# Performance work log

Hardware: AMD Instinct MI355X
Metric: run time of the kernel (lower is better)

The kernel has to match this reference:

```python
import jax, jax.numpy as jnp
import numpy as np
import math

B, S, H = 1, 2048, 4096
NH, HD = 32, 128  # heads, head_dim
ROPE_THETA = 10000.0
SINK = 4
RECENT_RATIO = 0.1


def setup_inputs() -> dict:
    key = jax.random.key(0)
    ks = jax.random.split(key, 5)
    scale = 0.02
    return {
        "hidden_states": jax.random.normal(ks[0], (B, S, H), jnp.float32),
        "Wq": jax.random.normal(ks[1], (H, H), jnp.float32) * scale,
        "Wk": jax.random.normal(ks[2], (H, H), jnp.float32) * scale,
        "Wv": jax.random.normal(ks[3], (H, H), jnp.float32) * scale,
        "Wo": jax.random.normal(ks[4], (H, H), jnp.float32) * scale,
        "position_ids": jnp.arange(S, dtype=jnp.int64)[None, :],
    }


def _rope(x, cos, sin):
    # x: [B, NH, S, HD]; rotate_half = cat(-x2, x1)
    half = x.shape[-1] // 2
    rot = jnp.concatenate([-x[..., half:], x[..., :half]], axis=-1)
    return x * cos + rot * sin


def reference(hidden_states, Wq, Wk, Wv, Wo, position_ids):
    b, s, h = hidden_states.shape
    # projections (torch Linear: x @ W^T), split heads -> [B, NH, S, HD]
    q = (hidden_states @ Wq.T).reshape(b, s, NH, HD).transpose(0, 2, 1, 3)
    k = (hidden_states @ Wk.T).reshape(b, s, NH, HD).transpose(0, 2, 1, 3)
    v = (hidden_states @ Wv.T).reshape(b, s, NH, HD).transpose(0, 2, 1, 3)

    # rotary embeddings from position_ids
    inv_freq = 1.0 / (ROPE_THETA ** (jnp.arange(0, HD, 2, dtype=jnp.float32) / HD))
    freqs = position_ids.astype(jnp.float32)[..., None] * inv_freq  # [B, S, HD/2]
    emb = jnp.concatenate([freqs, freqs], axis=-1)                   # [B, S, HD]
    cos = jnp.cos(emb)[:, None, :, :]
    sin = jnp.sin(emb)[:, None, :, :]
    q = _rope(q, cos, sin)
    k = _rope(k, cos, sin)

    # causal attention
    scores = jnp.einsum('bhqd,bhkd->bhqk', q, k) / math.sqrt(HD)
    neg = jnp.finfo(scores.dtype).min
    causal = jnp.tril(jnp.ones((s, s), dtype=bool))
    scores = jnp.where(causal[None, None], scores, neg)
    attn = jax.nn.softmax(scores, axis=-1)
    out = jnp.einsum('bhqk,bhkd->bhqd', attn, v)
    out = out.transpose(0, 2, 1, 3).reshape(b, s, h)
    attn_output = out @ Wo.T

    # H2O streaming cache eviction: sink (first 4) + recent window KV
    recent = int(s * RECENT_RATIO)
    k_evicted = jnp.concatenate([k[:, :, :SINK, :], k[:, :, s - recent:, :]], axis=2)
    v_evicted = jnp.concatenate([v[:, :, :SINK, :], v[:, :, s - recent:, :]], axis=2)
    return attn_output, k_evicted, v_evicted
```

## Files before the change

kernel.cpp:

```cpp
#include <hip/hip_runtime.h>
#include <hip/hip_bf16.h>

typedef __bf16 bf16;
typedef __bf16 bf16x4 __attribute__((ext_vector_type(4)));
typedef __bf16 bf16x8 __attribute__((ext_vector_type(8)));
typedef float f32x4 __attribute__((ext_vector_type(4)));

#define MFMA16(a, b, c) __builtin_amdgcn_mfma_f32_16x16x32_bf16(a, b, c, 0, 0, 0)

constexpr int S_LEN = 2048;
constexpr int HDIM = 4096;
constexpr int NHEADS = 32;
constexpr int HEADD = 128;
constexpr int SINKN = 4;
constexpr int RECENT = 204;
constexpr int EVROWS = SINKN + RECENT;
constexpr float QSCALE = 0.08838834764831845f;

constexpr int JOBS_PER_HEAD = 40;
constexpr int SLOTS_PER_HEAD = 36;
constexpr size_t SLOT_BYTES = 33792;

__device__ inline bf16x8 cvt8(const float* p) {
    float4 a = *(const float4*)p;
    float4 b = *(const float4*)(p + 4);
    return bf16x8{(bf16)a.x, (bf16)a.y, (bf16)a.z, (bf16)a.w,
                  (bf16)b.x, (bf16)b.y, (bf16)b.z, (bf16)b.w};
}

__device__ inline void gload16(const bf16* g, bf16* l) {
    __builtin_amdgcn_global_load_lds(
        (const __attribute__((address_space(1))) unsigned int*)g,
        (__attribute__((address_space(3))) unsigned int*)l, 16, 0, 0);
}

__global__ __launch_bounds__(256) void cvt_kernel(const float* __restrict__ in,
                                                  bf16* __restrict__ out, int n8) {
    int i = blockIdx.x * 256 + threadIdx.x;
    if (i >= n8) return;
    *(bf16x8*)(out + (size_t)i * 8) = cvt8(in + (size_t)i * 8);
}

__device__ __forceinline__ void stage128(const bf16* __restrict__ Ap,
                                         const bf16* __restrict__ Bp,
                                         bf16* Adst, bf16* Bdst,
                                         int K, int kc, int tid) {
#pragma unroll
    for (int r = 0; r < 2; ++r) {
        int idx = r * 512 + tid;
        int row = idx >> 3;
        int gs = (idx & 7) ^ (row & 7);
        gload16(Ap + (size_t)row * K + kc + gs * 8, Adst + idx * 8);
    }
#pragma unroll
    for (int r = 0; r < 2; ++r) {
        int idx = r * 512 + tid;
        int row = idx >> 3;
        int gs = (idx & 7) ^ (row & 7);
        gload16(Bp + (size_t)row * K + kc + gs * 8, Bdst + idx * 8);
    }
}
__device__ __forceinline__ void lda128(const bf16* buf, int wm, int lg, int lr,
                                       bf16x8 (&af)[2][2]) {
#pragma unroll
    for (int mt = 0; mt < 2; ++mt)
#pragma unroll
        for (int kk = 0; kk < 2; ++kk)
            af[mt][kk] = *(const bf16x8*)&buf[(wm * 32 + mt * 16 + lr) * 64 +
                                              (((kk * 4 + lg) ^ (lr & 7)) * 8)];
}
__device__ __forceinline__ void ldb128(const bf16* buf, int wn, int lg, int lr,
                                       bf16x8 (&bfr)[4][2]) {
#pragma unroll
    for (int nt = 0; nt < 4; ++nt)
#pragma unroll
        for (int kk = 0; kk < 2; ++kk)
            bfr[nt][kk] = *(const bf16x8*)&buf[(wn * 64 + nt * 16 + lr) * 64 +
                                               (((kk * 4 + lg) ^ (lr & 7)) * 8)];
}

template <bool C_IS_F32>
__global__ __launch_bounds__(512, 4) void gemm128(const bf16* __restrict__ A,
                                                  const bf16* __restrict__ B,
                                                  void* __restrict__ Cv,
                                                  int M, int N, int K) {
    __shared__ bf16 Abuf[2][128 * 64];
    __shared__ bf16 Bbuf[2][128 * 64];

    const int tid = threadIdx.x;
    const int lane = tid & 63, wid = tid >> 6;
    const int wm = wid >> 1, wn = wid & 1;
    const int lg = lane >> 4, lr = lane & 15;

    const int bid = blockIdx.x;
    const int xcd = bid & 7, wi = bid >> 3;
    const int bx = xcd * 4 + (wi >> 4);
    const int by = wi & 15;
    const int m0 = by * 128, n0 = bx * 128;

    const bf16* Ap = A + (size_t)m0 * K;
    const bf16* Bp = B + (size_t)n0 * K;

    f32x4 acc[2][4] = {};
    bf16x8 af[2][2], bfr[4][2];

    stage128(Ap, Bp, Abuf[0], Bbuf[0], K, 0, tid);

    int cur = 0;
    const int NT = K / 64;
    for (int t = 0; t < NT - 1; ++t) {
        stage128(Ap, Bp, Abuf[cur ^ 1], Bbuf[cur ^ 1], K, (t + 1) * 64, tid);
        asm volatile("s_waitcnt vmcnt(4)" ::: "memory");
        __builtin_amdgcn_s_barrier();
        __builtin_amdgcn_sched_barrier(0);

        lda128(Abuf[cur], wm, lg, lr, af);
        ldb128(Bbuf[cur], wn, lg, lr, bfr);
        asm volatile("s_waitcnt lgkmcnt(0)" ::: "memory");
        __builtin_amdgcn_sched_barrier(0);
        __builtin_amdgcn_s_setprio(1);
#pragma unroll
        for (int mt = 0; mt < 2; ++mt)
#pragma unroll
            for (int nt = 0; nt < 4; ++nt)
#pragma unroll
                for (int kk = 0; kk < 2; ++kk)
                    acc[mt][nt] = MFMA16(af[mt][kk], bfr[nt][kk], acc[mt][nt]);
        __builtin_amdgcn_s_setprio(0);
        __builtin_amdgcn_s_barrier();
        cur ^= 1;
    }
    asm volatile("s_waitcnt vmcnt(0)" ::: "memory");
    __builtin_amdgcn_s_barrier();
    lda128(Abuf[cur], wm, lg, lr, af);
    ldb128(Bbuf[cur], wn, lg, lr, bfr);
    asm volatile("s_waitcnt lgkmcnt(0)" ::: "memory");
    __builtin_amdgcn_sched_barrier(0);
#pragma unroll
    for (int mt = 0; mt < 2; ++mt)
#pragma unroll
        for (int nt = 0; nt < 4; ++nt)
#pragma unroll
            for (int kk = 0; kk < 2; ++kk)
                acc[mt][nt] = MFMA16(af[mt][kk], bfr[nt][kk], acc[mt][nt]);

#pragma unroll
    for (int mt = 0; mt < 2; ++mt)
#pragma unroll
        for (int nt = 0; nt < 4; ++nt)
#pragma unroll
            for (int r = 0; r < 4; ++r) {
                int row = m0 + wm * 32 + mt * 16 + lg * 4 + r;
                int col = n0 + wn * 64 + nt * 16 + lr;
                if constexpr (C_IS_F32)
                    ((float*)Cv)[(size_t)row * N + col] = acc[mt][nt][r];
                else
                    ((bf16*)Cv)[(size_t)row * N + col] = (bf16)acc[mt][nt][r];
            }
}

__global__ __launch_bounds__(256) void rope_kernel(bf16* __restrict__ q,
                                                   bf16* __restrict__ k) {
    const int s = blockIdx.x;
    const int t = threadIdx.x;
    const int hh = t >> 3;
    const int i0 = (t & 7) << 3;
    const size_t base = (size_t)s * HDIM + hh * HEADD;

    bf16x8 q1 = *(bf16x8*)(q + base + i0);
    bf16x8 q2 = *(bf16x8*)(q + base + 64 + i0);
    bf16x8 k1 = *(bf16x8*)(k + base + i0);
    bf16x8 k2 = *(bf16x8*)(k + base + 64 + i0);
    bf16x8 q1o, q2o, k1o, k2o;
    const float pos = (float)s;
#pragma unroll
    for (int j = 0; j < 8; ++j) {
        float f = pos * exp2f((float)(i0 + j) * (-0.2076205059304602f));
        float sn, cs;
        sincosf(f, &sn, &cs);
        float x1 = (float)q1[j], x2 = (float)q2[j];
        q1o[j] = (bf16)((x1 * cs - x2 * sn) * QSCALE);
        q2o[j] = (bf16)((x2 * cs + x1 * sn) * QSCALE);
        x1 = (float)k1[j]; x2 = (float)k2[j];
        k1o[j] = (bf16)(x1 * cs - x2 * sn);
        k2o[j] = (bf16)(x2 * cs + x1 * sn);
    }
    *(bf16x8*)(q + base + i0) = q1o;
    *(bf16x8*)(q + base + 64 + i0) = q2o;
    *(bf16x8*)(k + base + i0) = k1o;
    *(bf16x8*)(k + base + 64 + i0) = k2o;
}

__global__ __launch_bounds__(256) void transpose_v(const bf16* __restrict__ v,
                                                   bf16* __restrict__ vt) {
    __shared__ bf16 tile[64][136];
    const int h = blockIdx.x;
    const int s0 = blockIdx.y * 64;
    const int tid = threadIdx.x;
#pragma unroll
    for (int j = 0; j < 4; ++j) {
        int ch = tid + 256 * j;
        int row = ch >> 4, c8 = (ch & 15) << 3;
        *(bf16x8*)&tile[row][c8] =
            *(const bf16x8*)(v + (size_t)(s0 + row) * HDIM + h * HEADD + c8);
    }
    __syncthreads();
#pragma unroll
    for (int j = 0; j < 4; ++j) {
        int ch = tid + 256 * j;
        int d = ch >> 3, s8 = (ch & 7) << 3;
        bf16x8 w;
#pragma unroll
        for (int i = 0; i < 8; ++i) w[i] = tile[s8 + i][d];
        *(bf16x8*)(vt + ((size_t)h * HEADD + d) * S_LEN + s0 + s8) = w;
    }
}

__global__ __launch_bounds__(256, 2) void attn_kernel(const bf16* __restrict__ q,
                                                      const bf16* __restrict__ k,
                                                      const bf16* __restrict__ vt,
                                                      bf16* __restrict__ o,
                                                      char* __restrict__ partials) {
    __shared__ bf16 K_lds[2][64 * 128];
    __shared__ bf16 V_lds[128 * 64];
    __shared__ bf16 P_lds[4][32 * 72];

    const int tid = threadIdx.x;
    const int lane = tid & 63, wid = tid >> 6;
    const int lg = lane >> 4, lr = lane & 15;

    const int bj = blockIdx.x;
    const int h = bj / JOBS_PER_HEAD;
    const int within = JOBS_PER_HEAD - 1 - (bj % JOBS_PER_HEAD);
    int qb, chunk, nj;
    if (within < 4)       { qb = within; chunk = 0; nj = 1; }
    else if (within < 12) { int u2 = within - 4;  qb = 4  + (u2 >> 1); chunk = u2 & 1;        nj = 2; }
    else if (within < 24) { int u2 = within - 12; int q3 = u2 / 3; qb = 8 + q3; chunk = u2 - 3 * q3; nj = 3; }
    else                  { int u2 = within - 24; qb = 12 + (u2 >> 2); chunk = u2 & 3;        nj = 4; }
    const int q0 = qb * 128;
    const int ntiles = 2 * qb + 2;
    const int tb = chunk * 8;
    const int te = min(tb + 8, ntiles);

    bf16x8 aq[2][4];
#pragma unroll
    for (int rs = 0; rs < 2; ++rs)
#pragma unroll
        for (int dc = 0; dc < 4; ++dc)
            aq[rs][dc] = *(const bf16x8*)(q + (size_t)(q0 + wid * 32 + rs * 16 + lr) * HDIM +
                                          h * HEADD + dc * 32 + lg * 8);

    f32x4 oacc[2][8] = {};
    float m_[2] = {-1e30f, -1e30f};
    float l_[2] = {0.f, 0.f};
    bf16* pw = &P_lds[wid][0];

    {
        const int kv0 = tb << 6;
#pragma unroll
        for (int i = 0; i < 4; ++i) {
            const int c = wid * 4 + i;
            const int krow = 4 * c + (lane >> 4);
            const int kg = (lane & 15) ^ (krow & 7);
            gload16(k + (size_t)(kv0 + krow) * HDIM + h * HEADD + kg * 8,
                    &K_lds[0][c * 512]);
        }
    }

    int cur = 0;
    for (int t = tb; t < te; ++t) {
        const int kv0 = t << 6;
#pragma unroll
        for (int i = 0; i < 4; ++i) {
            const int c = wid * 4 + i;
            const int vrow = 8 * c + (lane >> 3);
            const int vg = (lane & 7) ^ (vrow & 7);
            gload16(vt + (size_t)(h * HEADD + vrow) * S_LEN + kv0 + vg * 8,
                    &V_lds[c * 512]);
        }
        if (t + 1 < te) {
            const int kvn = (t + 1) << 6;
#pragma unroll
            for (int i = 0; i < 4; ++i) {
                const int c = wid * 4 + i;
                const int krow = 4 * c + (lane >> 4);
                const int kg = (lane & 15) ^ (krow & 7);
                gload16(k + (size_t)(kvn + krow) * HDIM + h * HEADD + kg * 8,
                        &K_lds[cur ^ 1][c * 512]);
            }
            asm volatile("s_waitcnt vmcnt(8)" ::: "memory");
        } else {
            asm volatile("s_waitcnt vmcnt(4)" ::: "memory");
        }
        __builtin_amdgcn_s_barrier();
        __builtin_amdgcn_sched_barrier(0);

        const bf16* Kb = &K_lds[cur][0];
        f32x4 st[2][4] = {};
#pragma unroll
        for (int kt = 0; kt < 4; ++kt) {
            bf16x8 kf[4];
#pragma unroll
            for (int dc = 0; dc < 4; ++dc)
                kf[dc] = *(const bf16x8*)&Kb[(kt * 16 + lr) * 128 +
                                             (((dc * 4 + lg) ^ (lr & 7)) * 8)];
#pragma unroll
            for (int dc = 0; dc < 4; ++dc) {
                st[0][kt] = MFMA16(kf[dc], aq[0][dc], st[0][kt]);
                st[1][kt] = MFMA16(kf[dc], aq[1][dc], st[1][kt]);
            }
        }

#pragma unroll
        for (int rs = 0; rs < 2; ++rs) {
            const int qr0 = q0 + wid * 32 + rs * 16;
            const int qidx = qr0 + lr;
            const bool nm = (kv0 + 63) > qr0;
            float v[16];
#pragma unroll
            for (int kt = 0; kt < 4; ++kt)
#pragma unroll
                for (int r = 0; r < 4; ++r) {
                    float x = st[rs][kt][r];
                    if (nm && (kv0 + kt * 16 + lg * 4 + r > qidx)) x = -1e30f;
                    v[kt * 4 + r] = x;
                }
            float pm = v[0];
#pragma unroll
            for (int i = 1; i < 16; ++i) pm = fmaxf(pm, v[i]);
            pm = fmaxf(pm, __shfl_xor(pm, 16));
            pm = fmaxf(pm, __shfl_xor(pm, 32));

            if (__any(pm > m_[rs] + 8.0f)) {
                float mn = fmaxf(m_[rs], pm);
                float sc = __expf(m_[rs] - mn);
                m_[rs] = mn;
                l_[rs] *= sc;
                float scb[4];
#pragma unroll
                for (int r = 0; r < 4; ++r)
                    scb[r] = __uint_as_float(__builtin_amdgcn_ds_bpermute(
                        (lg * 4 + r) * 4, __float_as_uint(sc)));
#pragma unroll
                for (int dt = 0; dt < 8; ++dt)
#pragma unroll
                    for (int r = 0; r < 4; ++r) oacc[rs][dt][r] *= scb[r];
            }
            const float mn = m_[rs];
            float rsum = 0.f;
#pragma unroll
            for (int kt = 0; kt < 4; ++kt) {
                bf16x4 pk;
#pragma unroll
                for (int r = 0; r < 4; ++r) {
                    float p = __expf(v[kt * 4 + r] - mn);
                    rsum += p;
                    pk[r] = (bf16)p;
                }
                *(bf16x4*)&pw[(rs * 16 + lr) * 72 + kt * 16 + lg * 4] = pk;
            }
            rsum += __shfl_xor(rsum, 16);
            rsum += __shfl_xor(rsum, 32);
            l_[rs] += rsum;
        }

        if (t + 1 < te) asm volatile("s_waitcnt vmcnt(4)" ::: "memory");
        else            asm volatile("s_waitcnt vmcnt(0)" ::: "memory");
        __builtin_amdgcn_s_barrier();
        __builtin_amdgcn_sched_barrier(0);

        bf16x8 pa[2][2];
#pragma unroll
        for (int rs = 0; rs < 2; ++rs)
#pragma unroll
            for (int kt2 = 0; kt2 < 2; ++kt2)
                pa[rs][kt2] = *(const bf16x8*)&pw[(rs * 16 + lr) * 72 + kt2 * 32 + lg * 8];
#pragma unroll
        for (int kt2 = 0; kt2 < 2; ++kt2)
#pragma unroll
            for (int dt = 0; dt < 8; ++dt) {
                bf16x8 bv = *(const bf16x8*)&V_lds[(dt * 16 + lr) * 64 +
                                                   (((kt2 * 4 + lg) ^ (lr & 7)) * 8)];
                oacc[0][dt] = MFMA16(pa[0][kt2], bv, oacc[0][dt]);
                oacc[1][dt] = MFMA16(pa[1][kt2], bv, oacc[1][dt]);
            }

        __builtin_amdgcn_s_barrier();
        __builtin_amdgcn_sched_barrier(0);
        cur ^= 1;
    }

    if (nj == 1) {
#pragma unroll
        for (int rs = 0; rs < 2; ++rs) {
            float lb[4];
#pragma unroll
            for (int r = 0; r < 4; ++r)
                lb[r] = __uint_as_float(__builtin_amdgcn_ds_bpermute(
                    (lg * 4 + r) * 4, __float_as_uint(l_[rs])));
#pragma unroll
            for (int r = 0; r < 4; ++r) {
                float inv = 1.0f / lb[r];
                const int row = q0 + wid * 32 + rs * 16 + lg * 4 + r;
#pragma unroll
                for (int dt = 0; dt < 8; ++dt)
                    o[(size_t)row * HDIM + h * HEADD + dt * 16 + lr] =
                        (bf16)(oacc[rs][dt][r] * inv);
            }
        }
    } else {
        const int sb = (qb < 8) ? (qb - 4) * 2 : (qb < 12) ? 8 + (qb - 8) * 3
                                                           : 20 + (qb - 12) * 4;
        char* slotp = partials + ((size_t)h * SLOTS_PER_HEAD + sb + chunk) * SLOT_BYTES;
        bf16* Op = (bf16*)slotp;
        float* mp = (float*)(slotp + 32768);
        float* lp = mp + 128;
#pragma unroll
        for (int rs = 0; rs < 2; ++rs) {
            const int rowl = wid * 32 + rs * 16;
#pragma unroll
            for (int r = 0; r < 4; ++r)
#pragma unroll
                for (int dt = 0; dt < 8; ++dt)
                    Op[(rowl + lg * 4 + r) * HEADD + dt * 16 + lr] = (bf16)oacc[rs][dt][r];
            if (lg == 0) { mp[rowl + lr] = m_[rs]; lp[rowl + lr] = l_[rs]; }
        }
    }
}

__global__ __launch_bounds__(256) void combine_kernel(const char* __restrict__ partials,
                                                      bf16* __restrict__ o) {
    const int h = blockIdx.x;
    const int qb = 4 + blockIdx.y;
    const int nj = (2 * qb + 9) / 8;
    const int sb = (qb < 8) ? (qb - 4) * 2 : (qb < 12) ? 8 + (qb - 8) * 3
                                                       : 20 + (qb - 12) * 4;
    const char* base = partials + ((size_t)h * SLOTS_PER_HEAD + sb) * SLOT_BYTES;

    const int row = threadIdx.x >> 1;
    const int d0 = (threadIdx.x & 1) * 64;

    float mc[4], lc[4];
    float M = -1e30f;
    for (int c = 0; c < nj; ++c) {
        const char* sp = base + (size_t)c * SLOT_BYTES;
        mc[c] = ((const float*)(sp + 32768))[row];
        lc[c] = ((const float*)(sp + 33280))[row];
        M = fmaxf(M, mc[c]);
    }
    float denom = 0.f;
    float acc[64] = {};
    for (int c = 0; c < nj; ++c) {
        float wgt = __expf(mc[c] - M);
        denom += wgt * lc[c];
        const bf16* Op = (const bf16*)(base + (size_t)c * SLOT_BYTES);
#pragma unroll
        for (int j = 0; j < 8; ++j) {
            bf16x8 a = *(const bf16x8*)&Op[row * HEADD + d0 + j * 8];
#pragma unroll
            for (int e = 0; e < 8; ++e) acc[j * 8 + e] += wgt * (float)a[e];
        }
    }
    float inv = 1.0f / denom;
    bf16* dst = o + (size_t)(qb * 128 + row) * HDIM + h * HEADD + d0;
#pragma unroll
    for (int j = 0; j < 8; ++j) {
        bf16x8 w;
#pragma unroll
        for (int e = 0; e < 8; ++e) w[e] = (bf16)(acc[j * 8 + e] * inv);
        *(bf16x8*)&dst[j * 8] = w;
    }
}

__global__ __launch_bounds__(256) void evict_kernel(const bf16* __restrict__ k,
                                                    const bf16* __restrict__ v,
                                                    float* __restrict__ out) {
    const int total = NHEADS * EVROWS * HEADD;
    int idx = blockIdx.x * 256 + threadIdx.x;
    if (idx >= 2 * total) return;
    const int which = idx / total;
    const int rem = idx % total;
    const int hh = rem / (EVROWS * HEADD);
    const int i = (rem / HEADD) % EVROWS;
    const int d = rem % HEADD;
    const int s = (i < SINKN) ? i : (S_LEN - RECENT) + (i - SINKN);
    const bf16* src = which ? v : k;
    out[(size_t)S_LEN * HDIM + (size_t)which * total + rem] =
        (float)src[(size_t)s * HDIM + hh * HEADD + d];
}

extern "C" void kernel_launch(void* const* d_in, const int* in_sizes, int n_in,
                              void* d_out, int out_size, void* d_ws, size_t ws_size,
                              hipStream_t stream) {
    const float* hs = (const float*)d_in[0];
    const float* Wq = (const float*)d_in[1];
    const float* Wk = (const float*)d_in[2];
    const float* Wv = (const float*)d_in[3];
    const float* Wo = (const float*)d_in[4];
    float* out = (float*)d_out;

    const size_t MB = 1024 * 1024;
    char* w = (char*)d_ws;
    bf16* hs_bf = (bf16*)(w);
    bf16* W_bf  = (bf16*)(w + 16 * MB);
    char* part  = w;
    bf16* q_ws  = (bf16*)(w + 48 * MB);
    bf16* k_ws  = (bf16*)(w + 64 * MB);
    bf16* v_ws  = (bf16*)(w + 80 * MB);
    bf16* vt_ws = (bf16*)(w + 96 * MB);
    bf16* o_ws  = q_ws;

    const int nW8 = HDIM * HDIM / 8;
    const int nH8 = S_LEN * HDIM / 8;

    cvt_kernel<<<(nH8 + 255) / 256, 256, 0, stream>>>(hs, hs_bf, nH8);

    cvt_kernel<<<(nW8 + 255) / 256, 256, 0, stream>>>(Wq, W_bf, nW8);
    gemm128<false><<<512, 512, 0, stream>>>(hs_bf, W_bf, q_ws, S_LEN, HDIM, HDIM);
    cvt_kernel<<<(nW8 + 255) / 256, 256, 0, stream>>>(Wk, W_bf, nW8);
    gemm128<false><<<512, 512, 0, stream>>>(hs_bf, W_bf, k_ws, S_LEN, HDIM, HDIM);
    cvt_kernel<<<(nW8 + 255) / 256, 256, 0, stream>>>(Wv, W_bf, nW8);
    gemm128<false><<<512, 512, 0, stream>>>(hs_bf, W_bf, v_ws, S_LEN, HDIM, HDIM);

    rope_kernel<<<S_LEN, 256, 0, stream>>>(q_ws, k_ws);
    transpose_v<<<dim3(NHEADS, S_LEN / 64), 256, 0, stream>>>(v_ws, vt_ws);

    evict_kernel<<<(2 * NHEADS * EVROWS * HEADD + 255) / 256, 256, 0, stream>>>(k_ws, v_ws, out);

    attn_kernel<<<NHEADS * JOBS_PER_HEAD, 256, 0, stream>>>(q_ws, k_ws, vt_ws, o_ws, part);
    combine_kernel<<<dim3(NHEADS, 12), 256, 0, stream>>>(part, o_ws);

    cvt_kernel<<<(nW8 + 255) / 256, 256, 0, stream>>>(Wo, W_bf, nW8);
    gemm128<true><<<512, 512, 0, stream>>>(o_ws, W_bf, out, S_LEN, HDIM, HDIM);
}
```

Before: 455.4 us.

## Fuse fp32-to-bf16 weight conversion into GEMM B-operand loading

Removes the four separate weight conversion kernels. Each GEMM now reads fp32 weights straight from global memory into registers, converts them to bf16 and writes them to swizzled LDS, pipelined one k-tile ahead with adjusted vmcnt waits. This drops a full read and write pass over each 64MB weight matrix plus the bf16 re-read. In exchange the GEMM reads twice the B bytes, uses more registers (launch bounds lowered to 2 blocks), and does the conversion in VALU instructions inside the main loop.

```diff
diff --git a/kernel.cpp b/kernel.cpp
--- a/kernel.cpp
+++ b/kernel.cpp
@@ -28,6 +28,11 @@
                   (bf16)b.x, (bf16)b.y, (bf16)b.z, (bf16)b.w};
 }
 
+__device__ __forceinline__ bf16x8 cvt8f(const float4& a, const float4& b) {
+    return bf16x8{(bf16)a.x, (bf16)a.y, (bf16)a.z, (bf16)a.w,
+                  (bf16)b.x, (bf16)b.y, (bf16)b.z, (bf16)b.w};
+}
+
 __device__ inline void gload16(const bf16* g, bf16* l) {
     __builtin_amdgcn_global_load_lds(
         (const __attribute__((address_space(1))) unsigned int*)g,
@@ -41,10 +46,8 @@
     *(bf16x8*)(out + (size_t)i * 8) = cvt8(in + (size_t)i * 8);
 }
 
-__device__ __forceinline__ void stage128(const bf16* __restrict__ Ap,
-                                         const bf16* __restrict__ Bp,
-                                         bf16* Adst, bf16* Bdst,
-                                         int K, int kc, int tid) {
+__device__ __forceinline__ void stageA128(const bf16* __restrict__ Ap, bf16* Adst,
+                                          int K, int kc, int tid) {
 #pragma unroll
     for (int r = 0; r < 2; ++r) {
         int idx = r * 512 + tid;
@@ -52,13 +55,20 @@
         int gs = (idx & 7) ^ (row & 7);
         gload16(Ap + (size_t)row * K + kc + gs * 8, Adst + idx * 8);
     }
-#pragma unroll
-    for (int r = 0; r < 2; ++r) {
-        int idx = r * 512 + tid;
-        int row = idx >> 3;
-        int gs = (idx & 7) ^ (row & 7);
-        gload16(Bp + (size_t)row * K + kc + gs * 8, Bdst + idx * 8);
-    }
+}
+__device__ __forceinline__ void loadB_f32(const float* __restrict__ Bp, int K, int kc,
+                                          int tid, float4 (&br)[4]) {
+    const float* p = Bp + (size_t)(tid >> 2) * K + kc + (tid & 3) * 16;
+    br[0] = *(const float4*)p;
+    br[1] = *(const float4*)(p + 4);
+    br[2] = *(const float4*)(p + 8);
+    br[3] = *(const float4*)(p + 12);
+}
+__device__ __forceinline__ void writeB_lds(bf16* dst, int tid, const float4 (&br)[4]) {
+    const int row = tid >> 2;
+    const int c8 = (tid & 3) * 2;
+    *(bf16x8*)&dst[row * 64 + ((c8 ^ (row & 7)) * 8)] = cvt8f(br[0], br[1]);
+    *(bf16x8*)&dst[row * 64 + (((c8 + 1) ^ (row & 7)) * 8)] = cvt8f(br[2], br[3]);
 }
 __device__ __forceinline__ void lda128(const bf16* buf, int wm, int lg, int lr,
                                        bf16x8 (&af)[2][2]) {
@@ -80,10 +90,10 @@
 }
 
 template <bool C_IS_F32>
-__global__ __launch_bounds__(512, 4) void gemm128(const bf16* __restrict__ A,
-                                                  const bf16* __restrict__ B,
-                                                  void* __restrict__ Cv,
-                                                  int M, int N, int K) {
+__global__ __launch_bounds__(512, 2) void gemm128f(const bf16* __restrict__ A,
+                                                   const float* __restrict__ B,
+                                                   void* __restrict__ Cv,
+                                                   int M, int N, int K) {
     __shared__ bf16 Abuf[2][128 * 64];
     __shared__ bf16 Bbuf[2][128 * 64];
 
@@ -99,23 +109,41 @@
     const int m0 = by * 128, n0 = bx * 128;
 
     const bf16* Ap = A + (size_t)m0 * K;
-    const bf16* Bp = B + (size_t)n0 * K;
+    const float* Bp = B + (size_t)n0 * K;
 
     f32x4 acc[2][4] = {};
     bf16x8 af[2][2], bfr[4][2];
-
-    stage128(Ap, Bp, Abuf[0], Bbuf[0], K, 0, tid);
+    float4 br[4];
+
+    loadB_f32(Bp, K, 0, tid, br);
+    __builtin_amdgcn_sched_barrier(0);
+    stageA128(Ap, Abuf[0], K, 0, tid);
+    __builtin_amdgcn_sched_barrier(0);
+    asm volatile("s_waitcnt vmcnt(2)" ::: "memory");
+    writeB_lds(Bbuf[0], tid, br);
+    __builtin_amdgcn_sched_barrier(0);
+    loadB_f32(Bp, K, 64, tid, br);
+    __builtin_amdgcn_sched_barrier(0);
 
     int cur = 0;
     const int NT = K / 64;
     for (int t = 0; t < NT - 1; ++t) {
-        stage128(Ap, Bp, Abuf[cur ^ 1], Bbuf[cur ^ 1], K, (t + 1) * 64, tid);
-        asm volatile("s_waitcnt vmcnt(4)" ::: "memory");
+        stageA128(Ap, Abuf[cur ^ 1], K, (t + 1) * 64, tid);
+        __builtin_amdgcn_sched_barrier(0);
+        asm volatile("s_waitcnt vmcnt(6)" ::: "memory");
         __builtin_amdgcn_s_barrier();
         __builtin_amdgcn_sched_barrier(0);
 
         lda128(Abuf[cur], wm, lg, lr, af);
         ldb128(Bbuf[cur], wn, lg, lr, bfr);
+
+        asm volatile("s_waitcnt vmcnt(2)" ::: "memory");
+        writeB_lds(Bbuf[cur ^ 1], tid, br);
+        __builtin_amdgcn_sched_barrier(0);
+        if (t < NT - 2) {
+            loadB_f32(Bp, K, (t + 2) * 64, tid, br);
+            __builtin_amdgcn_sched_barrier(0);
+        }
         asm volatile("s_waitcnt lgkmcnt(0)" ::: "memory");
         __builtin_amdgcn_sched_barrier(0);
         __builtin_amdgcn_s_setprio(1);
@@ -502,7 +530,6 @@
     const size_t MB = 1024 * 1024;
     char* w = (char*)d_ws;
     bf16* hs_bf = (bf16*)(w);
-    bf16* W_bf  = (bf16*)(w + 16 * MB);
     char* part  = w;
     bf16* q_ws  = (bf16*)(w + 48 * MB);
     bf16* k_ws  = (bf16*)(w + 64 * MB);
@@ -510,17 +537,13 @@
     bf16* vt_ws = (bf16*)(w + 96 * MB);
     bf16* o_ws  = q_ws;
 
-    const int nW8 = HDIM * HDIM / 8;
     const int nH8 = S_LEN * HDIM / 8;
 
     cvt_kernel<<<(nH8 + 255) / 256, 256, 0, stream>>>(hs, hs_bf, nH8);
 
-    cvt_kernel<<<(nW8 + 255) / 256, 256, 0, stream>>>(Wq, W_bf, nW8);
-    gemm128<false><<<512, 512, 0, stream>>>(hs_bf, W_bf, q_ws, S_LEN, HDIM, HDIM);
-    cvt_kernel<<<(nW8 + 255) / 256, 256, 0, stream>>>(Wk, W_bf, nW8);
-    gemm128<false><<<512, 512, 0, stream>>>(hs_bf, W_bf, k_ws, S_LEN, HDIM, HDIM);
-    cvt_kernel<<<(nW8 + 255) / 256, 256, 0, stream>>>(Wv, W_bf, nW8);
-    gemm128<false><<<512, 512, 0, stream>>>(hs_bf, W_bf, v_ws, S_LEN, HDIM, HDIM);
+    gemm128f<false><<<512, 512, 0, stream>>>(hs_bf, Wq, q_ws, S_LEN, HDIM, HDIM);
+    gemm128f<false><<<512, 512, 0, stream>>>(hs_bf, Wk, k_ws, S_LEN, HDIM, HDIM);
+    gemm128f<false><<<512, 512, 0, stream>>>(hs_bf, Wv, v_ws, S_LEN, HDIM, HDIM);
 
     rope_kernel<<<S_LEN, 256, 0, stream>>>(q_ws, k_ws);
     transpose_v<<<dim3(NHEADS, S_LEN / 64), 256, 0, stream>>>(v_ws, vt_ws);
@@ -530,6 +553,5 @@
     attn_kernel<<<NHEADS * JOBS_PER_HEAD, 256, 0, stream>>>(q_ws, k_ws, vt_ws, o_ws, part);
     combine_kernel<<<dim3(NHEADS, 12), 256, 0, stream>>>(part, o_ws);
 
-    cvt_kernel<<<(nW8 + 255) / 256, 256, 0, stream>>>(Wo, W_bf, nW8);
-    gemm128<true><<<512, 512, 0, stream>>>(o_ws, W_bf, out, S_LEN, HDIM, HDIM);
-}
+    gemm128f<true><<<512, 512, 0, stream>>>(o_ws, Wo, out, S_LEN, HDIM, HDIM);
+}
```

Result: slower. 528.5 us (+16.1%).
